# Kernel tuning notes

Hardware: AMD Instinct MI355X
Metric: run time of the kernel (lower is better)

## Reference

```python
import jax, jax.numpy as jnp
import numpy as np

E = 512          # embed_dim
H = 8            # num_heads
FF = 2048        # ff_dim
MAX_LEN = 5000   # DynamicPositionalEncoding max_len
LN_EPS = 1e-5


def _layernorm(x, g, b):
    mu = jnp.mean(x, axis=-1, keepdims=True)
    var = jnp.mean((x - mu) ** 2, axis=-1, keepdims=True)
    return (x - mu) / jnp.sqrt(var + LN_EPS) * g + b


def setup_inputs() -> dict:
    key = jax.random.key(0)
    ks = jax.random.split(key, 12)
    S, B = 2048, 4
    s = 0.02
    return {
        "x": jax.random.normal(ks[0], (S, B, E), dtype=jnp.float32),
        "pos": jnp.zeros((1, MAX_LEN, E), dtype=jnp.float32),  # torch init: zeros Parameter
        "in_proj_w": jax.random.normal(ks[1], (3 * E, E), dtype=jnp.float32) * s,
        "in_proj_b": jnp.zeros((3 * E,), dtype=jnp.float32),
        "out_w": jax.random.normal(ks[2], (E, E), dtype=jnp.float32) * s,
        "out_b": jnp.zeros((E,), dtype=jnp.float32),
        "w1": jax.random.normal(ks[3], (FF, E), dtype=jnp.float32) * s,
        "b1": jnp.zeros((FF,), dtype=jnp.float32),
        "w2": jax.random.normal(ks[4], (E, FF), dtype=jnp.float32) * s,
        "b2": jnp.zeros((E,), dtype=jnp.float32),
        "g1": jnp.ones((E,), dtype=jnp.float32),
        "be1": jnp.zeros((E,), dtype=jnp.float32),
        "g2": jnp.ones((E,), dtype=jnp.float32),
        "be2": jnp.zeros((E,), dtype=jnp.float32),
        "local_window_size": 128,
    }


def reference(x, pos, in_proj_w, in_proj_b, out_w, out_b, w1, b1, w2, b2,
              g1, be1, g2, be2, local_window_size):
    S, B, _ = x.shape
    w = int(local_window_size)
    # quirk of original: pos encoding sliced by x.size(1) == batch, broadcast over seq
    x = x + pos[:, :B, :]

    # additive mask: local window [i-w, i+w] allowed, plus global columns every 2w
    i = jnp.arange(S)[:, None]
    j = jnp.arange(S)[None, :]
    allowed = (jnp.abs(i - j) <= w) | (j % (2 * w) == 0)
    mask = jnp.where(allowed, 0.0, -jnp.inf).astype(x.dtype)  # (S, S)

    # multihead self-attention (torch MHA semantics, seq-first)
    qkv = x @ in_proj_w.T + in_proj_b                 # (S, B, 3E)
    q, k, v = jnp.split(qkv, 3, axis=-1)
    hd = E // H

    def heads(t):  # (S, B, E) -> (B, H, S, hd)
        return t.reshape(S, B, H, hd).transpose(1, 2, 0, 3)

    q, k, v = heads(q), heads(k), heads(v)
    scale = 1.0 / jnp.sqrt(jnp.asarray(hd, x.dtype))
    scores = jnp.einsum("bhqd,bhkd->bhqk", q * scale, k) + mask
    attn = jax.nn.softmax(scores, axis=-1)
    y = jnp.einsum("bhqk,bhkd->bhqd", attn, v)        # (B, H, S, hd)
    y = y.transpose(2, 0, 1, 3).reshape(S, B, E)
    attn_out = y @ out_w.T + out_b

    x = _layernorm(x + attn_out, g1, be1)
    ff = jax.nn.relu(x @ w1.T + b1) @ w2.T + b2
    x = _layernorm(x + ff, g2, be2)
    return x
```

## Files before the change

### kernel.cpp

```cpp
#include <hip/hip_runtime.h>
#include <hip/hip_bf16.h>
#include <math.h>

#define S_LEN 2048
#define B_SZ  4
#define E_DIM 512
#define H_NUM 8
#define HD    64
#define FF_DIM 2048
#define NROWS 8192
#define WIN   128

typedef unsigned short u16;
typedef __bf16 bf16x8 __attribute__((ext_vector_type(8)));
typedef float  f32x4  __attribute__((ext_vector_type(4)));

__device__ __forceinline__ u16 f2bf(float f) {
  union { float f; unsigned u; } v; v.f = f;
  unsigned u = v.u;
  return (u16)((u + 0x7fffu + ((u >> 16) & 1u)) >> 16);
}

__device__ __forceinline__ void gl_lds16(const u16* gp, u16* lp) {
  __builtin_amdgcn_global_load_lds(
      (const __attribute__((address_space(1))) unsigned int*)gp,
      (__attribute__((address_space(3))) unsigned int*)lp, 16, 0, 0);
}

__global__ __launch_bounds__(256) void prep_kernel(
    const float* __restrict__ s0, const float* __restrict__ s1,
    const float* __restrict__ s2, const float* __restrict__ s3,
    u16* __restrict__ d0, u16* __restrict__ d1,
    u16* __restrict__ d2, u16* __restrict__ d3,
    const float* __restrict__ x, const float* __restrict__ pos,
    float* __restrict__ xp, u16* __restrict__ xpb) {
  int bx = blockIdx.x;
  if (bx < 3072) {
    const int n0 = 196608, n1 = 65536, n2 = 262144;
    int i = bx * blockDim.x + threadIdx.x;
    const float4* sp; ushort4* dp; int off;
    if (i < n0)                { sp = (const float4*)s0; dp = (ushort4*)d0; off = i; }
    else if (i < n0 + n1)      { sp = (const float4*)s1; dp = (ushort4*)d1; off = i - n0; }
    else if (i < n0 + n1 + n2) { sp = (const float4*)s2; dp = (ushort4*)d2; off = i - n0 - n1; }
    else                       { sp = (const float4*)s3; dp = (ushort4*)d3; off = i - n0 - n1 - n2; }
    float4 v = sp[off];
    ushort4 o; o.x = f2bf(v.x); o.y = f2bf(v.y); o.z = f2bf(v.z); o.w = f2bf(v.w);
    dp[off] = o;
  } else {
    int idx = (bx - 3072) * blockDim.x + threadIdx.x;
    float4 xv = ((const float4*)x)[idx];
    float4 pv = ((const float4*)pos)[idx & 511];
    float4 o;
    o.x = xv.x + pv.x; o.y = xv.y + pv.y; o.z = xv.z + pv.z; o.w = xv.w + pv.w;
    ((float4*)xp)[idx] = o;
    ushort4 ob; ob.x = f2bf(o.x); ob.y = f2bf(o.y); ob.z = f2bf(o.z); ob.w = f2bf(o.w);
    ((ushort4*)xpb)[idx] = ob;
  }
}

#define GBK 64

template <int BN, int GY>
__global__ __launch_bounds__(256) void mfma_gemm(
    const u16* __restrict__ A, const u16* __restrict__ W,
    const float* __restrict__ bias, float* __restrict__ outf,
    u16* __restrict__ outb, int M, int N, int K, int mode,
    u16* __restrict__ qb, u16* __restrict__ kb, u16* __restrict__ vb) {
  constexpr int TJ = BN / 32;
  __shared__ u16 SMEM[2 * 128 * GBK + 2 * BN * GBK];
  u16* As0 = SMEM;
  u16* Bs0 = SMEM + 2 * 128 * GBK;
  int tid = threadIdx.x;
  int lane = tid & 63;
  int w = tid >> 6;
  int lin = blockIdx.y * 64 + blockIdx.x;
  int xcd = lin & 7, slot = lin >> 3;
  int jj = slot % GY;
  int mm = (slot / GY) * 8 + xcd;
  int m0 = mm * 128;
  int j0 = jj * BN;
  int wrow = (w >> 1) * 64;
  int wcol = (w & 1) * (BN / 2);
  int lm = lane & 15;
  int kq = lane >> 4;
  int sw = lm & 7;
  int r8 = lane >> 3;
  int csrc = ((lane & 7) ^ r8) << 3;

  f32x4 acc[4][TJ];
#pragma unroll
  for (int i = 0; i < 4; i++)
#pragma unroll
    for (int j = 0; j < TJ; j++) acc[i][j] = (f32x4){0.f, 0.f, 0.f, 0.f};

  const u16* Ab = A + (size_t)m0 * K;
  const u16* Wb = W + (size_t)j0 * K;

  size_t soff[4];
#pragma unroll
  for (int u = 0; u < 4; u++)
    soff[u] = (size_t)(u * 32 + w * 8 + r8) * K + csrc;

  auto stage = [&](int kt, int pb) {
#pragma unroll
    for (int u = 0; u < 4; u++)
      gl_lds16(&Ab[soff[u] + kt], &As0[pb * 128 * GBK + (u * 4 + w) * 512]);
#pragma unroll
    for (int u = 0; u < TJ; u++)
      gl_lds16(&Wb[soff[u] + kt], &Bs0[pb * BN * GBK + (u * 4 + w) * 512]);
  };

  stage(0, 0);
  int pb = 0;
  for (int kt = 0; kt < K; kt += GBK) {
    __syncthreads();
    if (kt + GBK < K) stage(kt + GBK, pb ^ 1);
#pragma unroll
    for (int k2 = 0; k2 < GBK; k2 += 32) {
      int cc = ((((k2 >> 3) + kq) ^ sw) << 3);
      bf16x8 af[4], bfr[TJ];
#pragma unroll
      for (int t = 0; t < 4; t++)
        af[t] = *(const bf16x8*)&As0[pb * 128 * GBK + (wrow + t * 16 + lm) * GBK + cc];
#pragma unroll
      for (int tj = 0; tj < TJ; tj++)
        bfr[tj] = *(const bf16x8*)&Bs0[pb * BN * GBK + (wcol + tj * 16 + lm) * GBK + cc];
#pragma unroll
      for (int ti = 0; ti < 4; ti++)
#pragma unroll
        for (int tj = 0; tj < TJ; tj++)
          acc[ti][tj] = __builtin_amdgcn_mfma_f32_16x16x32_bf16(
              af[ti], bfr[tj], acc[ti][tj], 0, 0, 0);
    }
    pb ^= 1;
  }

  __syncthreads();
  if (mode == 0) {
    float* Cf = (float*)SMEM;
    constexpr int CF = BN + 4;
#pragma unroll
    for (int p = 0; p < 2; p++) {
      if ((w >> 1) == p) {
#pragma unroll
        for (int tj = 0; tj < TJ; tj++) {
          float bv = bias[j0 + wcol + tj * 16 + lm];
#pragma unroll
          for (int ti = 0; ti < 4; ti++)
#pragma unroll
            for (int r = 0; r < 4; r++)
              Cf[(ti * 16 + kq * 4 + r) * CF + wcol + tj * 16 + lm] =
                  acc[ti][tj][r] + bv;
        }
      }
      __syncthreads();
      constexpr int RC4 = BN / 4;
#pragma unroll
      for (int it = 0; it < 64 * RC4 / 256; it++) {
        int id = it * 256 + tid;
        int row = id / RC4, c4 = (id % RC4) * 4;
        float4 vq = *(float4*)&Cf[row * CF + c4];
        *(float4*)&outf[(size_t)(m0 + p * 64 + row) * N + j0 + c4] = vq;
      }
      __syncthreads();
    }
  } else {
    u16* Cs = (u16*)SMEM;
    constexpr int CS = BN + 8;
    int which = j0 >> 9;
    float qsc = (mode == 2 && which == 0) ? 0.125f : 1.f;
#pragma unroll
    for (int tj = 0; tj < TJ; tj++) {
      float bv = bias[j0 + wcol + tj * 16 + lm];
#pragma unroll
      for (int ti = 0; ti < 4; ti++)
#pragma unroll
        for (int r = 0; r < 4; r++) {
          float val = acc[ti][tj][r] + bv;
          if (mode == 1) val = fmaxf(val, 0.f);
          Cs[(wrow + ti * 16 + kq * 4 + r) * CS + wcol + tj * 16 + lm] =
              f2bf(val * qsc);
        }
    }
    __syncthreads();
    constexpr int RC8 = BN / 8;
#pragma unroll
    for (int it = 0; it < 128 * RC8 / 256; it++) {
      int id = it * 256 + tid;
      int row = id / RC8, c8 = (id % RC8) * 8;
      uint4 vq = *(uint4*)&Cs[row * CS + c8];
      if (mode == 1) {
        *(uint4*)&outb[(size_t)(m0 + row) * N + j0 + c8] = vq;
      } else {
        int e = (j0 & 511) + c8;
        int h = e >> 6, d0 = e & 63;
        int m = m0 + row, s = m >> 2, b = m & 3;
        u16* dst = (which == 0) ? qb : (which == 1) ? kb : vb;
        *(uint4*)&dst[((size_t)(b * H_NUM + h) * S_LEN + s) * HD + d0] = vq;
      }
    }
  }
}

__global__ __launch_bounds__(256) void attn_mfma_kernel(
    const u16* __restrict__ q, const u16* __restrict__ k,
    const u16* __restrict__ v, u16* __restrict__ yb) {
  __shared__ u16 Qs[64 * 64];
  __shared__ u16 Ks[64 * 64];
  __shared__ u16 Vs[64 * 64];
  __shared__ u16 Ps[64 * 64];
  int tid = threadIdx.x, lane = tid & 63, w = tid >> 6;
  int quad = lane >> 4, lm = lane & 15;
  int sw = lm & 7;
  int r8 = lane >> 3;
  int csrc = ((lane & 7) ^ r8) << 3;
  int lin = blockIdx.y * 32 + blockIdx.x;
  int xcd = lin & 7, slot = lin >> 3;
  int bh = xcd * 4 + (slot >> 5);
  int i0 = (slot & 31) * 64;
  int b = bh >> 3, h = bh & 7;
  const u16* qp = q + ((size_t)bh * S_LEN + i0) * HD;
  const u16* kp = k + (size_t)bh * S_LEN * HD;
  const u16* vp = v + (size_t)bh * S_LEN * HD;

#pragma unroll
  for (int u = 0; u < 2; u++) {
    int seg = u * 4 + w;
    int r = seg * 8 + r8;
    gl_lds16(&qp[(size_t)r * HD + csrc], &Qs[seg * 512]);
  }

  int cl = i0 - WIN; if (cl < 0) cl = 0;
  int chi = i0 + 63 + WIN; if (chi > S_LEN - 1) chi = S_LEN - 1;
  int nch = (chi - cl + 64) >> 6;
  int tlo = (cl + 255) >> 8;
  int thi0 = (chi >> 8) + 1;
  int ng = tlo + 8 - thi0;

  float m_i[4], l_i[4];
  f32x4 o[4];
#pragma unroll
  for (int r = 0; r < 4; r++) { m_i[r] = -INFINITY; l_i[r] = 0.f; }
#pragma unroll
  for (int tj = 0; tj < 4; tj++) o[tj] = (f32x4){0.f, 0.f, 0.f, 0.f};

  int arow = w * 16 + lm;
  int kpr = (arow & 7) ^ ((arow >> 2) & 7);

  for (int ch = 0; ch <= nch; ch++) {
    bool is_g = (ch == nch);
    int c0 = cl + (ch << 6);
    __syncthreads();
    if (!is_g) {
#pragma unroll
      for (int u = 0; u < 2; u++) {
        int seg = u * 4 + w;
        int r = seg * 8 + r8;
        gl_lds16(&kp[(size_t)(c0 + r) * HD + csrc], &Ks[seg * 512]);
      }
#pragma unroll
      for (int it = 0; it < 4; it++) {
        int flat = it * 256 + tid;
        int c = flat >> 4;
        int d0 = (flat & 15) << 2;
        ushort4 vv = make_ushort4(0, 0, 0, 0);
        int src = c0 + c;
        if (src <= chi) vv = *(const ushort4*)&vp[(size_t)src * HD + d0];
        u16 arr[4] = {vv.x, vv.y, vv.z, vv.w};
#pragma unroll
        for (int jd = 0; jd < 4; jd++) {
          int d = d0 + jd;
          int kd = (d & 7) ^ ((d >> 2) & 7);
          Vs[d * 64 + ((((c >> 3) ^ kd) << 3) | (c & 7))] = arr[jd];
        }
      }
    } else {
      if (w == 0) {
        int rr = lane >> 3;
        int grow = (rr < tlo) ? (rr << 8) : ((thi0 + rr - tlo) << 8);
        if (rr >= ng) grow = 0;
        gl_lds16(&kp[(size_t)grow * HD + (((lane & 7) ^ rr) << 3)], &Ks[0]);
      }
      for (int e = tid; e < 64 * 8; e += 256) {
        int d = e & 63, cg = e >> 6;
        if (cg < ng) {
          int gs = (cg < tlo) ? (cg << 8) : ((thi0 + cg - tlo) << 8);
          int kd = (d & 7) ^ ((d >> 2) & 7);
          Vs[d * 64 + (kd << 3) + cg] = vp[(size_t)gs * HD + d];
        }
      }
    }
    __syncthreads();

    f32x4 s[4];
#pragma unroll
    for (int tj = 0; tj < 4; tj++) s[tj] = (f32x4){0.f, 0.f, 0.f, 0.f};
    int tjn = is_g ? 1 : 4;
#pragma unroll
    for (int k2 = 0; k2 < 64; k2 += 32) {
      int cb = (k2 >> 3) + quad;
      bf16x8 a = *(const bf16x8*)&Qs[(w * 16 + lm) * 64 + ((cb ^ sw) << 3)];
      for (int tj = 0; tj < tjn; tj++) {
        bf16x8 bfr = *(const bf16x8*)&Ks[(tj * 16 + lm) * 64 + ((cb ^ sw) << 3)];
        s[tj] = __builtin_amdgcn_mfma_f32_16x16x32_bf16(a, bfr, s[tj], 0, 0, 0);
      }
    }
#pragma unroll
    for (int tj = 0; tj < 4; tj++) {
      int cidx = tj * 16 + lm;
      bool inval = is_g ? (cidx >= ng) : (c0 + cidx > chi);
      if (inval) {
        s[tj][0] = -INFINITY; s[tj][1] = -INFINITY;
        s[tj][2] = -INFINITY; s[tj][3] = -INFINITY;
      }
    }
#pragma unroll
    for (int r = 0; r < 4; r++) {
      float mx = fmaxf(fmaxf(s[0][r], s[1][r]), fmaxf(s[2][r], s[3][r]));
      mx = fmaxf(mx, __shfl_xor(mx, 1)); mx = fmaxf(mx, __shfl_xor(mx, 2));
      mx = fmaxf(mx, __shfl_xor(mx, 4)); mx = fmaxf(mx, __shfl_xor(mx, 8));
      float mnew = fmaxf(m_i[r], mx);
      float al = __expf(m_i[r] - mnew);
      float rs = 0.f;
#pragma unroll
      for (int tj = 0; tj < 4; tj++) {
        float p = __expf(s[tj][r] - mnew);
        s[tj][r] = p; rs += p;
      }
      rs += __shfl_xor(rs, 1); rs += __shfl_xor(rs, 2);
      rs += __shfl_xor(rs, 4); rs += __shfl_xor(rs, 8);
      l_i[r] = l_i[r] * al + rs;
      m_i[r] = mnew;
      o[0][r] *= al; o[1][r] *= al; o[2][r] *= al; o[3][r] *= al;
    }
#pragma unroll
    for (int tj = 0; tj < 4; tj++) {
      int cch = tj * 2 + (lm >> 3);
      int cof = lm & 7;
#pragma unroll
      for (int r = 0; r < 4; r++) {
        int row = w * 16 + quad * 4 + r;
        int kp2 = (row & 7) ^ ((row >> 2) & 7);
        Ps[row * 64 + ((cch ^ kp2) << 3) + cof] = f2bf(s[tj][r]);
      }
    }
    int kend = is_g ? 32 : 64;
#pragma unroll
    for (int k2 = 0; k2 < 64; k2 += 32) {
      if (k2 >= kend) break;
      int cb = (k2 >> 3) + quad;
      bf16x8 a = *(const bf16x8*)&Ps[arow * 64 + ((cb ^ kpr) << 3)];
#pragma unroll
      for (int tj = 0; tj < 4; tj++) {
        int vrow = tj * 16 + lm;
        int kv = (vrow & 7) ^ ((vrow >> 2) & 7);
        bf16x8 bfr = *(const bf16x8*)&Vs[vrow * 64 + ((cb ^ kv) << 3)];
        o[tj] = __builtin_amdgcn_mfma_f32_16x16x32_bf16(a, bfr, o[tj], 0, 0, 0);
      }
    }
  }

  __syncthreads();
#pragma unroll
  for (int r = 0; r < 4; r++) {
    float inv = 1.f / l_i[r];
    int row = w * 16 + quad * 4 + r;
    int kq2 = (row & 7) ^ ((row >> 2) & 7);
#pragma unroll
    for (int tj = 0; tj < 4; tj++) {
      int cch = tj * 2 + (lm >> 3);
      Qs[row * 64 + ((cch ^ kq2) << 3) + (lm & 7)] = f2bf(o[tj][r] * inv);
    }
  }
  __syncthreads();
#pragma unroll
  for (int it = 0; it < 2; it++) {
    int id = it * 256 + tid;
    int row = id >> 3, cch = id & 7;
    int kq2 = (row & 7) ^ ((row >> 2) & 7);
    uint4 vq = *(uint4*)&Qs[row * 64 + ((cch ^ kq2) << 3)];
    *(uint4*)&yb[((size_t)(i0 + row) * B_SZ + b) * E_DIM + h * HD + cch * 8] = vq;
  }
}

__global__ __launch_bounds__(256) void add_ln_kernel(
    const float* __restrict__ a, const float* __restrict__ r,
    const float* __restrict__ g, const float* __restrict__ be,
    float* __restrict__ out, u16* __restrict__ outb) {
  int wave = threadIdx.x >> 6;
  int lane = threadIdx.x & 63;
  int row = blockIdx.x * 4 + wave;
  const float* ar = a + (size_t)row * E_DIM;
  const float* rr = r + (size_t)row * E_DIM;
  float vals[8];
  float s = 0.f;
#pragma unroll
  for (int t = 0; t < 8; t++) {
    vals[t] = ar[t * 64 + lane] + rr[t * 64 + lane];
    s += vals[t];
  }
#pragma unroll
  for (int o = 32; o >= 1; o >>= 1) s += __shfl_xor(s, o, 64);
  float mu = s * (1.f / E_DIM);
  float vs = 0.f;
#pragma unroll
  for (int t = 0; t < 8; t++) { float d = vals[t] - mu; vs += d * d; }
#pragma unroll
  for (int o = 32; o >= 1; o >>= 1) vs += __shfl_xor(vs, o, 64);
  float inv = rsqrtf(vs * (1.f / E_DIM) + 1e-5f);
  float* orow = out + (size_t)row * E_DIM;
  u16* obrow = outb ? outb + (size_t)row * E_DIM : nullptr;
#pragma unroll
  for (int t = 0; t < 8; t++) {
    int e = t * 64 + lane;
    float val = (vals[t] - mu) * inv * g[e] + be[e];
    orow[e] = val;
    if (obrow) obrow[e] = f2bf(val);
  }
}

extern "C" void kernel_launch(void* const* d_in, const int* in_sizes, int n_in,
                              void* d_out, int out_size, void* d_ws, size_t ws_size,
                              hipStream_t stream) {
  const float* x     = (const float*)d_in[0];
  const float* pos   = (const float*)d_in[1];
  const float* in_w  = (const float*)d_in[2];
  const float* in_b  = (const float*)d_in[3];
  const float* out_w = (const float*)d_in[4];
  const float* out_b = (const float*)d_in[5];
  const float* w1    = (const float*)d_in[6];
  const float* b1    = (const float*)d_in[7];
  const float* w2    = (const float*)d_in[8];
  const float* b2    = (const float*)d_in[9];
  const float* g1    = (const float*)d_in[10];
  const float* be1   = (const float*)d_in[11];
  const float* g2    = (const float*)d_in[12];
  const float* be2   = (const float*)d_in[13];
  float* out = (float*)d_out;

  char* base = (char*)d_ws;
  float* xp    = (float*)(base);
  u16*   xpb   = (u16*)(base + ((size_t)16 << 20));
  u16*   qb    = (u16*)(base + ((size_t)24 << 20));
  u16*   kb    = (u16*)(base + ((size_t)32 << 20));
  u16*   vb    = (u16*)(base + ((size_t)40 << 20));
  u16*   ybf   = (u16*)(base + ((size_t)48 << 20));
  float* aprj  = (float*)(base + ((size_t)56 << 20));
  u16*   inwb  = (u16*)(base + ((size_t)72 << 20));
  u16*   outwb = (u16*)(base + ((size_t)74 << 20));
  u16*   w1b   = (u16*)(base + ((size_t)76 << 20));
  u16*   w2b   = (u16*)(base + ((size_t)78 << 20));
  float* x1    = xp;
  u16*   x1b   = xpb;
  u16*   ff1b  = qb;
  float* ff2   = aprj;

  prep_kernel<<<7168, 256, 0, stream>>>(in_w, out_w, w1, w2, inwb, outwb, w1b, w2b,
                                        x, pos, xp, xpb);
  mfma_gemm<128, 12><<<dim3(64, 12), 256, 0, stream>>>(xpb, inwb, in_b, nullptr, nullptr,
                                                       NROWS, 1536, 512, 2, qb, kb, vb);
  attn_mfma_kernel<<<dim3(32, 32), 256, 0, stream>>>(qb, kb, vb, ybf);
  mfma_gemm<64, 8><<<dim3(64, 8), 256, 0, stream>>>(ybf, outwb, out_b, aprj, nullptr,
                                                    NROWS, 512, 512, 0, nullptr, nullptr, nullptr);
  add_ln_kernel<<<2048, 256, 0, stream>>>(xp, aprj, g1, be1, x1, x1b);
  mfma_gemm<128, 16><<<dim3(64, 16), 256, 0, stream>>>(x1b, w1b, b1, nullptr, ff1b,
                                                       NROWS, 2048, 512, 1, nullptr, nullptr, nullptr);
  mfma_gemm<64, 8><<<dim3(64, 8), 256, 0, stream>>>(ff1b, w2b, b2, ff2, nullptr,
                                                    NROWS, 512, 2048, 0, nullptr, nullptr, nullptr);
  add_ln_kernel<<<2048, 256, 0, stream>>>(x1, ff2, g2, be2, out, nullptr);
}
```

Baseline: 253.5 us.

## Pre-transpose V and double-buffer K/V tiles in local attention kernel

Adds a separate kernel that transposes V into a (bh, d, s) layout ahead of attention. The attention kernel can then stage V with async global-to-LDS loads like K instead of a scalar scatter-transpose. K and V shared tiles are double-buffered so the next chunk loads while the current one computes. This costs an extra kernel launch, an extra pass over V in memory, and twice the LDS for K/V, which may lower occupancy.

```diff
diff --git a/kernel.cpp b/kernel.cpp
--- a/kernel.cpp
+++ b/kernel.cpp
@@ -202,12 +202,45 @@
   }
 }
 
+__global__ __launch_bounds__(256) void vtrans_kernel(
+    const u16* __restrict__ vb, u16* __restrict__ vtb) {
+  __shared__ u16 Ts[64 * 64];
+  int tid = threadIdx.x;
+  int lin = blockIdx.x;
+  int bh = lin >> 5, s0 = (lin & 31) * 64;
+  const u16* src = vb + ((size_t)bh * S_LEN + s0) * HD;
+#pragma unroll
+  for (int it = 0; it < 4; it++) {
+    int flat = it * 256 + tid;
+    int c = flat >> 4;
+    int d0 = (flat & 15) << 2;
+    ushort4 vv = *(const ushort4*)&src[(size_t)c * HD + d0];
+    u16 arr[4] = {vv.x, vv.y, vv.z, vv.w};
+#pragma unroll
+    for (int jd = 0; jd < 4; jd++) {
+      int d = d0 + jd;
+      int kd = (d & 7) ^ ((d >> 2) & 7);
+      Ts[d * 64 + ((((c >> 3) ^ kd) << 3) | (c & 7))] = arr[jd];
+    }
+  }
+  __syncthreads();
+  u16* dst = vtb + (size_t)bh * HD * S_LEN + s0;
+#pragma unroll
+  for (int it = 0; it < 2; it++) {
+    int id = it * 256 + tid;
+    int row = id >> 3, cch = id & 7;
+    int kd = (row & 7) ^ ((row >> 2) & 7);
+    uint4 vq = *(uint4*)&Ts[row * 64 + ((cch ^ kd) << 3)];
+    *(uint4*)&dst[(size_t)row * S_LEN + cch * 8] = vq;
+  }
+}
+
 __global__ __launch_bounds__(256) void attn_mfma_kernel(
     const u16* __restrict__ q, const u16* __restrict__ k,
-    const u16* __restrict__ v, u16* __restrict__ yb) {
+    const u16* __restrict__ vt, u16* __restrict__ yb) {
   __shared__ u16 Qs[64 * 64];
-  __shared__ u16 Ks[64 * 64];
-  __shared__ u16 Vs[64 * 64];
+  __shared__ u16 Ks[2][64 * 64];
+  __shared__ u16 Vs[2][64 * 64];
   __shared__ u16 Ps[64 * 64];
   int tid = threadIdx.x, lane = tid & 63, w = tid >> 6;
   int quad = lane >> 4, lm = lane & 15;
@@ -221,7 +254,7 @@
   int b = bh >> 3, h = bh & 7;
   const u16* qp = q + ((size_t)bh * S_LEN + i0) * HD;
   const u16* kp = k + (size_t)bh * S_LEN * HD;
-  const u16* vp = v + (size_t)bh * S_LEN * HD;
+  const u16* vp = vt + (size_t)bh * HD * S_LEN;
 
 #pragma unroll
   for (int u = 0; u < 2; u++) {
@@ -237,60 +270,50 @@
   int thi0 = (chi >> 8) + 1;
   int ng = tlo + 8 - thi0;
 
-  float m_i[4], l_i[4];
-  f32x4 o[4];
-#pragma unroll
-  for (int r = 0; r < 4; r++) { m_i[r] = -INFINITY; l_i[r] = 0.f; }
-#pragma unroll
-  for (int tj = 0; tj < 4; tj++) o[tj] = (f32x4){0.f, 0.f, 0.f, 0.f};
-
-  int arow = w * 16 + lm;
-  int kpr = (arow & 7) ^ ((arow >> 2) & 7);
-
-  for (int ch = 0; ch <= nch; ch++) {
-    bool is_g = (ch == nch);
-    int c0 = cl + (ch << 6);
-    __syncthreads();
-    if (!is_g) {
+  auto stageKV = [&](int ch, int buf) {
+    if (ch < nch) {
+      int c0 = cl + (ch << 6);
 #pragma unroll
       for (int u = 0; u < 2; u++) {
         int seg = u * 4 + w;
         int r = seg * 8 + r8;
-        gl_lds16(&kp[(size_t)(c0 + r) * HD + csrc], &Ks[seg * 512]);
-      }
-#pragma unroll
-      for (int it = 0; it < 4; it++) {
-        int flat = it * 256 + tid;
-        int c = flat >> 4;
-        int d0 = (flat & 15) << 2;
-        ushort4 vv = make_ushort4(0, 0, 0, 0);
-        int src = c0 + c;
-        if (src <= chi) vv = *(const ushort4*)&vp[(size_t)src * HD + d0];
-        u16 arr[4] = {vv.x, vv.y, vv.z, vv.w};
-#pragma unroll
-        for (int jd = 0; jd < 4; jd++) {
-          int d = d0 + jd;
-          int kd = (d & 7) ^ ((d >> 2) & 7);
-          Vs[d * 64 + ((((c >> 3) ^ kd) << 3) | (c & 7))] = arr[jd];
-        }
+        gl_lds16(&kp[(size_t)(c0 + r) * HD + csrc], &Ks[buf][seg * 512]);
+        gl_lds16(&vp[(size_t)r * S_LEN + c0 + csrc], &Vs[buf][seg * 512]);
       }
     } else {
       if (w == 0) {
         int rr = lane >> 3;
         int grow = (rr < tlo) ? (rr << 8) : ((thi0 + rr - tlo) << 8);
         if (rr >= ng) grow = 0;
-        gl_lds16(&kp[(size_t)grow * HD + (((lane & 7) ^ rr) << 3)], &Ks[0]);
+        gl_lds16(&kp[(size_t)grow * HD + (((lane & 7) ^ rr) << 3)], &Ks[buf][0]);
       }
       for (int e = tid; e < 64 * 8; e += 256) {
         int d = e & 63, cg = e >> 6;
         if (cg < ng) {
           int gs = (cg < tlo) ? (cg << 8) : ((thi0 + cg - tlo) << 8);
-          int kd = (d & 7) ^ ((d >> 2) & 7);
-          Vs[d * 64 + (kd << 3) + cg] = vp[(size_t)gs * HD + d];
+          Vs[buf][d * 64 + ((d & 7) << 3) + cg] = vp[(size_t)d * S_LEN + gs];
         }
       }
     }
+  };
+
+  float m_i[4], l_i[4];
+  f32x4 o[4];
+#pragma unroll
+  for (int r = 0; r < 4; r++) { m_i[r] = -INFINITY; l_i[r] = 0.f; }
+#pragma unroll
+  for (int tj = 0; tj < 4; tj++) o[tj] = (f32x4){0.f, 0.f, 0.f, 0.f};
+
+  int arow = w * 16 + lm;
+  int kpr = (arow & 7) ^ ((arow >> 2) & 7);
+
+  stageKV(0, 0);
+  for (int ch = 0; ch <= nch; ch++) {
+    bool is_g = (ch == nch);
+    int c0 = cl + (ch << 6);
+    int buf = ch & 1;
     __syncthreads();
+    if (ch < nch) stageKV(ch + 1, buf ^ 1);
 
     f32x4 s[4];
 #pragma unroll
@@ -301,7 +324,7 @@
       int cb = (k2 >> 3) + quad;
       bf16x8 a = *(const bf16x8*)&Qs[(w * 16 + lm) * 64 + ((cb ^ sw) << 3)];
       for (int tj = 0; tj < tjn; tj++) {
-        bf16x8 bfr = *(const bf16x8*)&Ks[(tj * 16 + lm) * 64 + ((cb ^ sw) << 3)];
+        bf16x8 bfr = *(const bf16x8*)&Ks[buf][(tj * 16 + lm) * 64 + ((cb ^ sw) << 3)];
         s[tj] = __builtin_amdgcn_mfma_f32_16x16x32_bf16(a, bfr, s[tj], 0, 0, 0);
       }
     }
@@ -352,9 +375,7 @@
       bf16x8 a = *(const bf16x8*)&Ps[arow * 64 + ((cb ^ kpr) << 3)];
 #pragma unroll
       for (int tj = 0; tj < 4; tj++) {
-        int vrow = tj * 16 + lm;
-        int kv = (vrow & 7) ^ ((vrow >> 2) & 7);
-        bf16x8 bfr = *(const bf16x8*)&Vs[vrow * 64 + ((cb ^ kv) << 3)];
+        bf16x8 bfr = *(const bf16x8*)&Vs[buf][(tj * 16 + lm) * 64 + ((cb ^ sw) << 3)];
         o[tj] = __builtin_amdgcn_mfma_f32_16x16x32_bf16(a, bfr, o[tj], 0, 0, 0);
       }
     }
@@ -450,6 +471,7 @@
   u16*   outwb = (u16*)(base + ((size_t)74 << 20));
   u16*   w1b   = (u16*)(base + ((size_t)76 << 20));
   u16*   w2b   = (u16*)(base + ((size_t)78 << 20));
+  u16*   vtb   = xpb;
   float* x1    = xp;
   u16*   x1b   = xpb;
   u16*   ff1b  = qb;
@@ -459,7 +481,8 @@
                                         x, pos, xp, xpb);
   mfma_gemm<128, 12><<<dim3(64, 12), 256, 0, stream>>>(xpb, inwb, in_b, nullptr, nullptr,
                                                        NROWS, 1536, 512, 2, qb, kb, vb);
-  attn_mfma_kernel<<<dim3(32, 32), 256, 0, stream>>>(qb, kb, vb, ybf);
+  vtrans_kernel<<<1024, 256, 0, stream>>>(vb, vtb);
+  attn_mfma_kernel<<<dim3(32, 32), 256, 0, stream>>>(qb, kb, vtb, ybf);
   mfma_gemm<64, 8><<<dim3(64, 8), 256, 0, stream>>>(ybf, outwb, out_b, aprj, nullptr,
                                                     NROWS, 512, 512, 0, nullptr, nullptr, nullptr);
   add_ln_kernel<<<2048, 256, 0, stream>>>(xp, aprj, g1, be1, x1, x1b);
```

New measurement: 251.0 us. No clear change (-1.0%).
